# Optimization experiments

Measured on AMD Instinct MI355X. Metric: run time of the kernel, lower is better.

The kernel has to match this reference:

```python
import jax, jax.numpy as jnp
import numpy as np

N = 50000      # nodes
R = 4          # relations
E = 150000     # edges per relation
IN_DIM = 128
HID_DIM = 128
OUT_DIM = 128


def setup_inputs() -> dict:
    key = jax.random.key(0)
    ks = jax.random.split(key, 8)
    x = jax.random.normal(ks[0], (N, IN_DIM), dtype=jnp.float32)
    edge_src = jax.random.randint(ks[1], (R, E), 0, N, dtype=jnp.int32)
    edge_dst = jax.random.randint(ks[2], (R, E), 0, N, dtype=jnp.int32)
    # Glorot-ish init for per-relation GraphConv weights, zero biases (DGL default).
    W1 = jax.random.normal(ks[3], (R, IN_DIM, HID_DIM), dtype=jnp.float32) / np.sqrt(IN_DIM)
    b1 = jnp.zeros((R, HID_DIM), dtype=jnp.float32)
    W2 = jax.random.normal(ks[4], (R, HID_DIM, OUT_DIM), dtype=jnp.float32) / np.sqrt(HID_DIM)
    b2 = jnpp = jnp.zeros((R, OUT_DIM), dtype=jnp.float32)
    return {"x": x, "edge_src": edge_src, "edge_dst": edge_dst,
            "W1": W1, "b1": b1, "W2": W2, "b2": b2}


def _hetero_conv(h, edge_src, edge_dst, W, b):
    """HeteroGraphConv(sum) over R relations, each a DGL GraphConv(norm='both').

    GraphConv: out = D_in^{-1/2} * scatter_sum(D_out^{-1/2} * h[src] -> dst) @ W + b
    with degrees clamped to >= 1.
    """
    n = h.shape[0]

    def rel_conv(src, dst, Wr, br):
        ones = jnp.ones(src.shape, dtype=h.dtype)
        deg_out = jnp.maximum(jax.ops.segment_sum(ones, src, num_segments=n), 1.0)
        deg_in = jnp.maximum(jax.ops.segment_sum(ones, dst, num_segments=n), 1.0)
        hn = h * jax.lax.rsqrt(deg_out)[:, None]          # [N, d] source-side norm
        msg = jnp.take(hn, src, axis=0)                    # [E, d] gather
        agg = jax.ops.segment_sum(msg, dst, num_segments=n)  # [N, d] scatter-sum
        agg = agg * jax.lax.rsqrt(deg_in)[:, None]         # dest-side norm
        return agg @ Wr + br                               # [N, d_out]

    out_per_rel = jax.vmap(rel_conv)(edge_src, edge_dst, W, b)  # [R, N, d_out]
    return out_per_rel.sum(axis=0)                               # sum-aggregate across relations


def reference(x, edge_src, edge_dst, W1, b1, W2, b2):
    h = _hetero_conv(x, edge_src, edge_dst, W1, b1)
    h = jax.nn.relu(h)
    out = _hetero_conv(h, edge_src, edge_dst, W2, b2)
    return out
```

## Files before the change

kernel.cpp:

```cpp
#include <hip/hip_runtime.h>
#include <hip/hip_bf16.h>
#include <stdint.h>

#define N_NODES 50000
#define R_REL   4
#define E_EDGES 150000
#define E_TOT   600000
#define DIM     128
#define K_TOT   512
#define M_PAD   50048
#define NB      200000
#define CAP     24
#define BM      64
#define BK      64
#define EBLK    2344
#define PBLK    512
#define XBLK    3125
#define ZBLK    391

typedef __attribute__((ext_vector_type(4))) float f32x4;
typedef __attribute__((ext_vector_type(8))) short short8;
typedef __attribute__((ext_vector_type(4))) short s16x4;
typedef __attribute__((ext_vector_type(4))) int i32x4;

__device__ __forceinline__ short f2bf(float f) {
    union { float f; unsigned u; } x{f};
    unsigned r = (x.u + 0x7fffu + ((x.u >> 16) & 1u)) >> 16;
    return (short)r;
}
__device__ __forceinline__ float bf2f(short s) {
    union { unsigned u; float f; } x;
    x.u = ((unsigned)(unsigned short)s) << 16;
    return x.f;
}

__global__ void zero_ws(int* __restrict__ p) {
    int i = blockIdx.x * 256 + threadIdx.x;
    i32x4 z = {0, 0, 0, 0};
    if ((size_t)i * 4 < 2 * NB) *((i32x4*)p + i) = z;
}

__global__ void prep_all(const int* __restrict__ src,
                         int* __restrict__ cnt_src,
                         const float* __restrict__ x, short* __restrict__ xb,
                         const float* __restrict__ W1, const float* __restrict__ b1,
                         const float* __restrict__ W2, const float* __restrict__ b2,
                         short* __restrict__ Wt1, short* __restrict__ Wt2,
                         float* __restrict__ bias1, float* __restrict__ bias2) {
    if (blockIdx.x < EBLK) {
        int i = blockIdx.x * 256 + threadIdx.x;
        if (i >= E_TOT) return;
        int r = i / E_EDGES;
        atomicAdd(&cnt_src[src[i] * 4 + r], 1);
    } else if (blockIdx.x < EBLK + XBLK) {
        size_t i = (size_t)(blockIdx.x - EBLK) * 2048 + threadIdx.x * 8;
        f32x4 a = *(const f32x4*)(x + i);
        f32x4 b = *(const f32x4*)(x + i + 4);
        short8 o;
        o[0] = f2bf(a[0]); o[1] = f2bf(a[1]); o[2] = f2bf(a[2]); o[3] = f2bf(a[3]);
        o[4] = f2bf(b[0]); o[5] = f2bf(b[1]); o[6] = f2bf(b[2]); o[7] = f2bf(b[3]);
        *(short8*)(xb + i) = o;
    } else {
        int i = (blockIdx.x - EBLK - XBLK) * 256 + threadIdx.x;
        int layer = i >= DIM * K_TOT;
        int j = i - layer * DIM * K_TOT;
        const float* W = layer ? W2 : W1;
        short* Wt = layer ? Wt2 : Wt1;
        int o = j / K_TOT, k = j % K_TOT;
        Wt[j] = f2bf(W[(size_t)k * DIM + o]);
        if (j < DIM) {
            const float* b = layer ? b2 : b1;
            float* bias = layer ? bias2 : bias1;
            float s = 0.f;
            for (int r = 0; r < R_REL; ++r) s += b[r * DIM + j];
            bias[j] = s;
        }
    }
}

__global__ void fill_binned(const int* __restrict__ src, const int* __restrict__ dst,
                            const int* __restrict__ cnt_src,
                            int* __restrict__ deg_cur, int2* __restrict__ binned) {
    int i = blockIdx.x * 256 + threadIdx.x;
    if (i >= E_TOT) return;
    int r = i / E_EDGES;
    int s = src[i], d = dst[i];
    int b = d * 4 + r;
    int rank = atomicAdd(&deg_cur[b], 1);
    if (rank < CAP) {
        float w = rsqrtf(fmaxf((float)cnt_src[s * 4 + r], 1.0f));
        int2 rec;
        rec.x = s;
        rec.y = __float_as_int(w);
        binned[b * CAP + rank] = rec;
    }
}

__global__ void gather_edges(const int* __restrict__ deg_cur, const int2* __restrict__ binned,
                             const short* __restrict__ h, short* __restrict__ agg) {
    int t = blockIdx.x * blockDim.x + threadIdx.x;
    int d = t >> 5;
    if (d >= N_NODES) return;
    int lane = t & 31;
    int p0 = d * 4;

    int4 dg = *(const int4*)(deg_cur + p0);
    int degs[4] = {dg.x, dg.y, dg.z, dg.w};
    int cnt_[4];
#pragma unroll
    for (int k = 0; k < 4; ++k) cnt_[k] = degs[k] < CAP ? degs[k] : CAP;

    int   sidx[4][4];
    float wv[4][4];
#pragma unroll
    for (int k = 0; k < 4; ++k) {
        const int2* base = binned + (p0 + k) * CAP;
        int4 qa = *(const int4*)base;
        int4 qb = *(const int4*)(base + 2);
        int   sx[4] = {qa.x, qa.z, qb.x, qb.z};
        int   sw[4] = {qa.y, qa.w, qb.y, qb.w};
#pragma unroll
        for (int j = 0; j < 4; ++j) {
            bool m = j < cnt_[k];
            sidx[k][j] = m ? sx[j] : 0;
            wv[k][j]   = m ? __int_as_float(sw[j]) : 0.f;
        }
    }

    s16x4 v[4][4];
#pragma unroll
    for (int k = 0; k < 4; ++k)
#pragma unroll
        for (int j = 0; j < 4; ++j)
            v[k][j] = *((const s16x4*)(h + (size_t)sidx[k][j] * DIM) + lane);

    f32x4 acc[4] = {};
#pragma unroll
    for (int k = 0; k < 4; ++k)
#pragma unroll
        for (int j = 0; j < 4; ++j) {
            f32x4 fv;
            fv[0] = bf2f(v[k][j][0]); fv[1] = bf2f(v[k][j][1]);
            fv[2] = bf2f(v[k][j][2]); fv[3] = bf2f(v[k][j][3]);
            acc[k] += fv * wv[k][j];
        }

#pragma unroll
    for (int k = 0; k < 4; ++k) {
        for (int e0 = 4; e0 < cnt_[k]; e0 += 4) {
            const int2* base = binned + (p0 + k) * CAP + e0;
            int4 qa = *(const int4*)base;
            int4 qb = *(const int4*)(base + 2);
            int sx[4] = {qa.x, qa.z, qb.x, qb.z};
            int sw[4] = {qa.y, qa.w, qb.y, qb.w};
#pragma unroll
            for (int j = 0; j < 4; ++j) {
                bool m = e0 + j < cnt_[k];
                int   si = m ? sx[j] : 0;
                float w  = m ? __int_as_float(sw[j]) : 0.f;
                s16x4 u = *((const s16x4*)(h + (size_t)si * DIM) + lane);
                f32x4 fu;
                fu[0] = bf2f(u[0]); fu[1] = bf2f(u[1]);
                fu[2] = bf2f(u[2]); fu[3] = bf2f(u[3]);
                acc[k] += fu * w;
            }
        }
    }

#pragma unroll
    for (int k = 0; k < 4; ++k) {
        float rs = rsqrtf(fmaxf((float)degs[k], 1.0f));
        f32x4 a = acc[k] * rs;
        s16x4 o;
        o[0] = f2bf(a[0]); o[1] = f2bf(a[1]); o[2] = f2bf(a[2]); o[3] = f2bf(a[3]);
        *((s16x4*)(agg + (size_t)d * K_TOT + k * DIM) + lane) = o;
    }
}

template <bool RELU, bool OUTBF>
__global__ __launch_bounds__(256, 4)
void gemm_kernel(const short* __restrict__ A, const short* __restrict__ Wt,
                 const float* __restrict__ bias, void* __restrict__ outv) {
    __shared__ short a_sh[64 * 72];
    __shared__ short b_sh[128 * 72];

    const int tid  = threadIdx.x;
    const int bm0  = blockIdx.x * BM;
    const int lane = tid & 63;
    const int wid  = tid >> 6;
    const int wm   = wid >> 1, wn = wid & 1;
    const int l15  = lane & 15, l4 = lane >> 4;

    f32x4 acc[2][4] = {};

    for (int kk = 0; kk < K_TOT; kk += BK) {
        __syncthreads();
#pragma unroll
        for (int j = 0; j < 2; ++j) {
            int c = tid + 256 * j;
            int row = c >> 3, ku = c & 7;
            *(short8*)&a_sh[row * 72 + ku * 8] =
                *(const short8*)(A + (size_t)(bm0 + row) * K_TOT + kk + ku * 8);
        }
#pragma unroll
        for (int j = 0; j < 4; ++j) {
            int c = tid + 256 * j;
            int col = c >> 3, ku = c & 7;
            *(short8*)&b_sh[col * 72 + ku * 8] =
                *(const short8*)(Wt + (size_t)col * K_TOT + kk + ku * 8);
        }
        __syncthreads();
#pragma unroll
        for (int ki = 0; ki < 2; ++ki) {
            short8 a[2], b[4];
            int ku = ki * 4 + l4;
#pragma unroll
            for (int f = 0; f < 2; ++f) {
                int row = wm * 32 + f * 16 + l15;
                a[f] = *(const short8*)&a_sh[row * 72 + ku * 8];
            }
#pragma unroll
            for (int f = 0; f < 4; ++f) {
                int col = wn * 64 + f * 16 + l15;
                b[f] = *(const short8*)&b_sh[col * 72 + ku * 8];
            }
#pragma unroll
            for (int fm = 0; fm < 2; ++fm)
#pragma unroll
                for (int fn = 0; fn < 4; ++fn)
                    acc[fm][fn] = __builtin_amdgcn_mfma_f32_16x16x32_bf16(
                        a[fm], b[fn], acc[fm][fn], 0, 0, 0);
        }
    }

#pragma unroll
    for (int fn = 0; fn < 4; ++fn) {
        int col = wn * 64 + fn * 16 + l15;
        float bi = bias[col];
#pragma unroll
        for (int fm = 0; fm < 2; ++fm) {
            int row0 = bm0 + wm * 32 + fm * 16 + l4 * 4;
#pragma unroll
            for (int rr = 0; rr < 4; ++rr) {
                int row = row0 + rr;
                if (row < N_NODES) {
                    float v = acc[fm][fn][rr] + bi;
                    if (RELU) v = fmaxf(v, 0.f);
                    if (OUTBF) ((short*)outv)[(size_t)row * DIM + col] = f2bf(v);
                    else       ((float*)outv)[(size_t)row * DIM + col] = v;
                }
            }
        }
    }
}

extern "C" void kernel_launch(void* const* d_in, const int* in_sizes, int n_in,
                              void* d_out, int out_size, void* d_ws, size_t ws_size,
                              hipStream_t stream) {
    const float* x    = (const float*)d_in[0];
    const int*   esrc = (const int*)  d_in[1];
    const int*   edst = (const int*)  d_in[2];
    const float* W1   = (const float*)d_in[3];
    const float* b1   = (const float*)d_in[4];
    const float* W2   = (const float*)d_in[5];
    const float* b2   = (const float*)d_in[6];
    float* out = (float*)d_out;
    char*  ws  = (char*)d_ws;

    float* bias1   = (float*)(ws + 0);
    float* bias2   = (float*)(ws + 512);
    short* Wt1     = (short*)(ws + 1024);
    short* Wt2     = (short*)(ws + 132096);
    short* xb      = (short*)(ws + 263168);
    short* h       = (short*)(ws + 13063168);
    short* agg     = (short*)(ws + 25863168);
    int*   cnt_src = (int*)  (ws + 77112320);
    int*   deg_cur = (int*)  (ws + 77912320);
    int2*  binned  = (int2*) (ws + 78712320);

    zero_ws<<<ZBLK, 256, 0, stream>>>(cnt_src);

    prep_all<<<EBLK + XBLK + PBLK, 256, 0, stream>>>(esrc, cnt_src, x, xb,
                                                     W1, b1, W2, b2,
                                                     Wt1, Wt2, bias1, bias2);

    fill_binned<<<EBLK, 256, 0, stream>>>(esrc, edst, cnt_src, deg_cur, binned);

    const int gat_blocks = (N_NODES * 32 + 255) / 256;
    const int gemm_blocks = M_PAD / BM;

    gather_edges<<<gat_blocks, 256, 0, stream>>>(deg_cur, binned, xb, agg);
    gemm_kernel<true, true><<<gemm_blocks, 256, 0, stream>>>(agg, Wt1, bias1, h);

    gather_edges<<<gat_blocks, 256, 0, stream>>>(deg_cur, binned, h, agg);
    gemm_kernel<false, false><<<gemm_blocks, 256, 0, stream>>>(agg, Wt2, bias2, out);
}
```

Measured before the change: 174.4 us.

## Fuse edge gather with per-block GEMM, keeping aggregated rows in LDS

The separate gather and GEMM kernels are merged into one fused_layer kernel per layer. Each 32-row block gathers its neighbour aggregates for all four relations straight into shared memory (row stride 520), then runs MFMA against the staged weight tiles. This removes the global round trip of the large bf16 agg buffer and one launch per layer. In exchange, each block carries about 51 KB of LDS, the launch-bounds occupancy target drops from 4 to 3, and weight tiles are reloaded by twice as many blocks. The padded tail rows need zeroed degree entries, so the zeroing range is extended.

```diff
diff --git a/kernel.cpp b/kernel.cpp
--- a/kernel.cpp
+++ b/kernel.cpp
@@ -10,13 +10,15 @@
 #define K_TOT   512
 #define M_PAD   50048
 #define NB      200000
+#define NPAD    192
 #define CAP     24
-#define BM      64
+#define BM      32
 #define BK      64
 #define EBLK    2344
 #define PBLK    512
 #define XBLK    3125
 #define ZBLK    391
+#define LDA     520
 
 typedef __attribute__((ext_vector_type(4))) float f32x4;
 typedef __attribute__((ext_vector_type(8))) short short8;
@@ -37,7 +39,7 @@
 __global__ void zero_ws(int* __restrict__ p) {
     int i = blockIdx.x * 256 + threadIdx.x;
     i32x4 z = {0, 0, 0, 0};
-    if ((size_t)i * 4 < 2 * NB) *((i32x4*)p + i) = z;
+    if (i * 4 < 2 * NB + NPAD) *((i32x4*)p + i) = z;
 }
 
 __global__ void prep_all(const int* __restrict__ src,
@@ -96,112 +98,106 @@
     }
 }
 
-__global__ void gather_edges(const int* __restrict__ deg_cur, const int2* __restrict__ binned,
-                             const short* __restrict__ h, short* __restrict__ agg) {
-    int t = blockIdx.x * blockDim.x + threadIdx.x;
-    int d = t >> 5;
-    if (d >= N_NODES) return;
-    int lane = t & 31;
-    int p0 = d * 4;
-
-    int4 dg = *(const int4*)(deg_cur + p0);
-    int degs[4] = {dg.x, dg.y, dg.z, dg.w};
-    int cnt_[4];
-#pragma unroll
-    for (int k = 0; k < 4; ++k) cnt_[k] = degs[k] < CAP ? degs[k] : CAP;
-
-    int   sidx[4][4];
-    float wv[4][4];
-#pragma unroll
-    for (int k = 0; k < 4; ++k) {
-        const int2* base = binned + (p0 + k) * CAP;
-        int4 qa = *(const int4*)base;
-        int4 qb = *(const int4*)(base + 2);
-        int   sx[4] = {qa.x, qa.z, qb.x, qb.z};
-        int   sw[4] = {qa.y, qa.w, qb.y, qb.w};
-#pragma unroll
-        for (int j = 0; j < 4; ++j) {
-            bool m = j < cnt_[k];
-            sidx[k][j] = m ? sx[j] : 0;
-            wv[k][j]   = m ? __int_as_float(sw[j]) : 0.f;
-        }
-    }
-
-    s16x4 v[4][4];
-#pragma unroll
-    for (int k = 0; k < 4; ++k)
-#pragma unroll
-        for (int j = 0; j < 4; ++j)
-            v[k][j] = *((const s16x4*)(h + (size_t)sidx[k][j] * DIM) + lane);
-
-    f32x4 acc[4] = {};
-#pragma unroll
-    for (int k = 0; k < 4; ++k)
-#pragma unroll
-        for (int j = 0; j < 4; ++j) {
-            f32x4 fv;
-            fv[0] = bf2f(v[k][j][0]); fv[1] = bf2f(v[k][j][1]);
-            fv[2] = bf2f(v[k][j][2]); fv[3] = bf2f(v[k][j][3]);
-            acc[k] += fv * wv[k][j];
-        }
-
-#pragma unroll
-    for (int k = 0; k < 4; ++k) {
-        for (int e0 = 4; e0 < cnt_[k]; e0 += 4) {
-            const int2* base = binned + (p0 + k) * CAP + e0;
+template <bool RELU, bool OUTBF>
+__global__ __launch_bounds__(256, 3)
+void fused_layer(const int* __restrict__ deg_cur, const int2* __restrict__ binned,
+                 const short* __restrict__ h, const short* __restrict__ Wt,
+                 const float* __restrict__ bias, void* __restrict__ outv) {
+    __shared__ short a_sh[BM * LDA];
+    __shared__ short b_sh[128 * 72];
+
+    const int tid  = threadIdx.x;
+    const int bm0  = blockIdx.x * BM;
+    const int lane = tid & 31;
+    const int g    = tid >> 5;
+
+    for (int jn = 0; jn < 4; ++jn) {
+        int row = g * 4 + jn;
+        int p0 = (bm0 + row) * 4;
+
+        int4 dg = *(const int4*)(deg_cur + p0);
+        int degs[4] = {dg.x, dg.y, dg.z, dg.w};
+        int cnt_[4];
+#pragma unroll
+        for (int k = 0; k < 4; ++k) cnt_[k] = degs[k] < CAP ? degs[k] : CAP;
+
+        int   sidx[4][4];
+        float wv[4][4];
+#pragma unroll
+        for (int k = 0; k < 4; ++k) {
+            const int2* base = binned + (size_t)(p0 + k) * CAP;
             int4 qa = *(const int4*)base;
             int4 qb = *(const int4*)(base + 2);
             int sx[4] = {qa.x, qa.z, qb.x, qb.z};
             int sw[4] = {qa.y, qa.w, qb.y, qb.w};
 #pragma unroll
             for (int j = 0; j < 4; ++j) {
-                bool m = e0 + j < cnt_[k];
-                int   si = m ? sx[j] : 0;
-                float w  = m ? __int_as_float(sw[j]) : 0.f;
-                s16x4 u = *((const s16x4*)(h + (size_t)si * DIM) + lane);
-                f32x4 fu;
-                fu[0] = bf2f(u[0]); fu[1] = bf2f(u[1]);
-                fu[2] = bf2f(u[2]); fu[3] = bf2f(u[3]);
-                acc[k] += fu * w;
-            }
-        }
-    }
-
-#pragma unroll
-    for (int k = 0; k < 4; ++k) {
-        float rs = rsqrtf(fmaxf((float)degs[k], 1.0f));
-        f32x4 a = acc[k] * rs;
-        s16x4 o;
-        o[0] = f2bf(a[0]); o[1] = f2bf(a[1]); o[2] = f2bf(a[2]); o[3] = f2bf(a[3]);
-        *((s16x4*)(agg + (size_t)d * K_TOT + k * DIM) + lane) = o;
-    }
-}
-
-template <bool RELU, bool OUTBF>
-__global__ __launch_bounds__(256, 4)
-void gemm_kernel(const short* __restrict__ A, const short* __restrict__ Wt,
-                 const float* __restrict__ bias, void* __restrict__ outv) {
-    __shared__ short a_sh[64 * 72];
-    __shared__ short b_sh[128 * 72];
-
-    const int tid  = threadIdx.x;
-    const int bm0  = blockIdx.x * BM;
-    const int lane = tid & 63;
-    const int wid  = tid >> 6;
-    const int wm   = wid >> 1, wn = wid & 1;
-    const int l15  = lane & 15, l4 = lane >> 4;
-
-    f32x4 acc[2][4] = {};
+                bool m = j < cnt_[k];
+                sidx[k][j] = m ? sx[j] : 0;
+                wv[k][j]   = m ? __int_as_float(sw[j]) : 0.f;
+            }
+        }
+
+        s16x4 v[4][4];
+#pragma unroll
+        for (int k = 0; k < 4; ++k)
+#pragma unroll
+            for (int j = 0; j < 4; ++j)
+                v[k][j] = *((const s16x4*)(h + (size_t)sidx[k][j] * DIM) + lane);
+
+        f32x4 acc[4] = {};
+#pragma unroll
+        for (int k = 0; k < 4; ++k)
+#pragma unroll
+            for (int j = 0; j < 4; ++j) {
+                f32x4 fv;
+                fv[0] = bf2f(v[k][j][0]); fv[1] = bf2f(v[k][j][1]);
+                fv[2] = bf2f(v[k][j][2]); fv[3] = bf2f(v[k][j][3]);
+                acc[k] += fv * wv[k][j];
+            }
+
+#pragma unroll
+        for (int k = 0; k < 4; ++k) {
+            for (int e0 = 4; e0 < cnt_[k]; e0 += 4) {
+                const int2* base = binned + (size_t)(p0 + k) * CAP + e0;
+                int4 qa = *(const int4*)base;
+                int4 qb = *(const int4*)(base + 2);
+                int sx[4] = {qa.x, qa.z, qb.x, qb.z};
+                int sw[4] = {qa.y, qa.w, qb.y, qb.w};
+#pragma unroll
+                for (int j = 0; j < 4; ++j) {
+                    bool m = e0 + j < cnt_[k];
+                    int   si = m ? sx[j] : 0;
+                    float w  = m ? __int_as_float(sw[j]) : 0.f;
+                    s16x4 u = *((const s16x4*)(h + (size_t)si * DIM) + lane);
+                    f32x4 fu;
+                    fu[0] = bf2f(u[0]); fu[1] = bf2f(u[1]);
+                    fu[2] = bf2f(u[2]); fu[3] = bf2f(u[3]);
+                    acc[k] += fu * w;
+                }
+            }
+        }
+
+#pragma unroll
+        for (int k = 0; k < 4; ++k) {
+            float rs = rsqrtf(fmaxf((float)degs[k], 1.0f));
+            f32x4 a = acc[k] * rs;
+            s16x4 o;
+            o[0] = f2bf(a[0]); o[1] = f2bf(a[1]); o[2] = f2bf(a[2]); o[3] = f2bf(a[3]);
+            *((s16x4*)&a_sh[row * LDA + k * DIM] + lane) = o;
+        }
+    }
+    __syncthreads();
+
+    const int lane64 = tid & 63;
+    const int wid = tid >> 6;
+    const int wm = wid >> 1, wn = wid & 1;
+    const int l15 = lane64 & 15, l4 = lane64 >> 4;
+
+    f32x4 acc[4] = {};
 
     for (int kk = 0; kk < K_TOT; kk += BK) {
-        __syncthreads();
-#pragma unroll
-        for (int j = 0; j < 2; ++j) {
-            int c = tid + 256 * j;
-            int row = c >> 3, ku = c & 7;
-            *(short8*)&a_sh[row * 72 + ku * 8] =
-                *(const short8*)(A + (size_t)(bm0 + row) * K_TOT + kk + ku * 8);
-        }
+        if (kk) __syncthreads();
 #pragma unroll
         for (int j = 0; j < 4; ++j) {
             int c = tid + 256 * j;
@@ -212,24 +208,15 @@
         __syncthreads();
 #pragma unroll
         for (int ki = 0; ki < 2; ++ki) {
-            short8 a[2], b[4];
             int ku = ki * 4 + l4;
-#pragma unroll
-            for (int f = 0; f < 2; ++f) {
-                int row = wm * 32 + f * 16 + l15;
-                a[f] = *(const short8*)&a_sh[row * 72 + ku * 8];
-            }
-#pragma unroll
-            for (int f = 0; f < 4; ++f) {
-                int col = wn * 64 + f * 16 + l15;
-                b[f] = *(const short8*)&b_sh[col * 72 + ku * 8];
-            }
-#pragma unroll
-            for (int fm = 0; fm < 2; ++fm)
-#pragma unroll
-                for (int fn = 0; fn < 4; ++fn)
-                    acc[fm][fn] = __builtin_amdgcn_mfma_f32_16x16x32_bf16(
-                        a[fm], b[fn], acc[fm][fn], 0, 0, 0);
+            short8 a_ = *(const short8*)&a_sh[(wm * 16 + l15) * LDA + kk + ku * 8];
+            short8 b_[4];
+#pragma unroll
+            for (int f = 0; f < 4; ++f)
+                b_[f] = *(const short8*)&b_sh[(wn * 64 + f * 16 + l15) * 72 + ku * 8];
+#pragma unroll
+            for (int fn = 0; fn < 4; ++fn)
+                acc[fn] = __builtin_amdgcn_mfma_f32_16x16x32_bf16(a_, b_[fn], acc[fn], 0, 0, 0);
         }
     }
 
@@ -237,18 +224,15 @@
     for (int fn = 0; fn < 4; ++fn) {
         int col = wn * 64 + fn * 16 + l15;
         float bi = bias[col];
-#pragma unroll
-        for (int fm = 0; fm < 2; ++fm) {
-            int row0 = bm0 + wm * 32 + fm * 16 + l4 * 4;
-#pragma unroll
-            for (int rr = 0; rr < 4; ++rr) {
-                int row = row0 + rr;
-                if (row < N_NODES) {
-                    float v = acc[fm][fn][rr] + bi;
-                    if (RELU) v = fmaxf(v, 0.f);
-                    if (OUTBF) ((short*)outv)[(size_t)row * DIM + col] = f2bf(v);
-                    else       ((float*)outv)[(size_t)row * DIM + col] = v;
-                }
+        int row0 = bm0 + wm * 16 + l4 * 4;
+#pragma unroll
+        for (int rr = 0; rr < 4; ++rr) {
+            int row = row0 + rr;
+            if (row < N_NODES) {
+                float v = acc[fn][rr] + bi;
+                if (RELU) v = fmaxf(v, 0.f);
+                if (OUTBF) ((short*)outv)[(size_t)row * DIM + col] = f2bf(v);
+                else       ((float*)outv)[(size_t)row * DIM + col] = v;
             }
         }
     }
@@ -273,10 +257,9 @@
     short* Wt2     = (short*)(ws + 132096);
     short* xb      = (short*)(ws + 263168);
     short* h       = (short*)(ws + 13063168);
-    short* agg     = (short*)(ws + 25863168);
-    int*   cnt_src = (int*)  (ws + 77112320);
-    int*   deg_cur = (int*)  (ws + 77912320);
-    int2*  binned  = (int2*) (ws + 78712320);
+    int*   cnt_src = (int*)  (ws + 25863168);
+    int*   deg_cur = (int*)  (ws + 26663168);
+    int2*  binned  = (int2*) (ws + 27463936);
 
     zero_ws<<<ZBLK, 256, 0, stream>>>(cnt_src);
 
@@ -286,12 +269,9 @@
 
     fill_binned<<<EBLK, 256, 0, stream>>>(esrc, edst, cnt_src, deg_cur, binned);
 
-    const int gat_blocks = (N_NODES * 32 + 255) / 256;
-    const int gemm_blocks = M_PAD / BM;
-
-    gather_edges<<<gat_blocks, 256, 0, stream>>>(deg_cur, binned, xb, agg);
-    gemm_kernel<true, true><<<gemm_blocks, 256, 0, stream>>>(agg, Wt1, bias1, h);
-
-    gather_edges<<<gat_blocks, 256, 0, stream>>>(deg_cur, binned, h, agg);
-    gemm_kernel<false, false><<<gemm_blocks, 256, 0, stream>>>(agg, Wt2, bias2, out);
-}
+    const int blocks = M_PAD / BM;
+
+    fused_layer<true, true><<<blocks, 256, 0, stream>>>(deg_cur, binned, xb, Wt1, bias1, h);
+
+    fused_layer<false, false><<<blocks, 256, 0, stream>>>(deg_cur, binned, h, Wt2, bias2, out);
+}
```

Result: slower. 183.9 us (+5.5%).
